# Kernel optimization log

Measured on AMD Instinct MI355X. Metric: run time of the kernel, lower is better.

Reference implementation:

```python
import jax
import jax.numpy as jnp
import numpy as np

B, L = 64, 128


def _lse(x, axis):
    # -inf-safe logsumexp; mirrors the torch code's NaN-masking autograd hooks
    m = jax.lax.stop_gradient(jnp.max(x, axis=axis, keepdims=True))
    m = jnp.where(jnp.isfinite(m), m, 0.0)
    s = jnp.sum(jnp.exp(x - m), axis=axis)
    out = jnp.log(jnp.where(s > 0, s, 1.0)) + jnp.squeeze(m, axis=axis)
    return jnp.where(s > 0, out, -jnp.inf)


def _inside(scores_p, lens):
    # scores_p: [L, L, B] == torch scores.permute(2, 1, 0); Eisner inside algorithm
    L_, _, Bn = scores_p.shape
    ar = jnp.arange(L_)
    ninf = jnp.array(-jnp.inf, scores_p.dtype)
    s_i = jnp.full((L_, L_, Bn), -jnp.inf, scores_p.dtype)  # incomplete spans
    s_c = jnp.full((L_, L_, Bn), -jnp.inf, scores_p.dtype)  # complete spans
    s_c = s_c.at[ar, ar].set(0.0)

    def step(carry, w):
        s_i, s_c = carry
        i = ar[:, None]                      # span start
        j = ar[None, :]                      # split offset
        valid = (j < w) & (i < L_ - w)       # [L, L] stripe mask for width w
        clip = lambda x: jnp.clip(x, 0, L_ - 1)
        vi = (ar < L_ - w)[:, None]          # valid span starts, [L, 1]
        lo, hi = clip(ar + w), ar            # diagonal coords (i+w, i)

        # incomplete: I(i<->i+w) = lse_r C(i, i+r) + C(i+w, i+r+1)  (stripe + stripe(w,1))
        ilr = s_c[clip(i), clip(i + j)] + s_c[clip(i + w), clip(i + j + 1)]
        il = _lse(jnp.where(valid[..., None], ilr, ninf), 1)       # [L, B]
        s_i = s_i.at[lo, hi].set(jnp.where(vi, il + scores_p[lo, hi], s_i[lo, hi]))
        s_i = s_i.at[hi, lo].set(jnp.where(vi, il + scores_p[hi, lo], s_i[hi, lo]))

        # complete left: C(i+w -> i) = lse_r C(i+r, i) + I(i+w, i+r)
        cl = s_c[clip(i + j), clip(i)] + s_i[clip(i + w), clip(i + j)]
        clv = _lse(jnp.where(valid[..., None], cl, ninf), 1)
        s_c = s_c.at[lo, hi].set(jnp.where(vi, clv, s_c[lo, hi]))

        # complete right: C(i -> i+w) = lse_r I(i, i+r+1) + C(i+r+1, i+w)
        cr = s_i[clip(i), clip(i + j + 1)] + s_c[clip(i + j + 1), clip(i + w)]
        crv = _lse(jnp.where(valid[..., None], cr, ninf), 1)
        # root span (0, w) is only valid for sentences of exactly length w
        crv = crv.at[0].set(jnp.where(lens == w, crv[0], ninf))
        s_c = s_c.at[hi, lo].set(jnp.where(vi, crv, s_c[hi, lo]))
        return (s_i, s_c), None

    (s_i, s_c), _ = jax.lax.scan(jax.checkpoint(step), (s_i, s_c), jnp.arange(1, L_))
    return s_i, s_c


def setup_inputs() -> dict:
    key = jax.random.key(0)
    k1, k2, k3 = jax.random.split(key, 3)
    scores = jax.random.normal(k1, (B, L, L), jnp.float32)
    lens = jax.random.randint(k2, (B,), L // 2, L)                 # sentence lengths
    pos = jnp.arange(L)
    mask = (pos[None, :] >= 1) & (pos[None, :] <= lens[:, None])   # prefix mask, mask.sum(1)==lens
    target = jax.random.randint(k3, (B, L), 0, L)
    target = jnp.minimum(target, lens[:, None])                    # gold heads inside sentence
    return {"scores": scores, "mask": mask, "target": target}


def reference(scores, mask, target):
    Bn, L_, _ = scores.shape
    lens = mask.sum(1)
    total = mask.sum().astype(scores.dtype)
    s_i, s_c = _inside(jnp.transpose(scores, (2, 1, 0)), lens)
    logZ = s_c[0, lens, jnp.arange(Bn)].sum()
    gold = jnp.take_along_axis(scores, target[..., None], axis=-1)[..., 0]
    loss = (logZ - jnp.where(mask, gold, jnp.zeros((), scores.dtype)).sum()) / total
    return loss
```

## Files before the change

kernel.cpp:

```cpp
#include <hip/hip_runtime.h>
#include <math.h>

#define LL 128
#define LP 129
#define TCR 132
#define TC_SZ (TCR * LP)
#define TI_SZ (LL * LP + 160)
#define NT 512
#define NW 8

#define LOG2E 1.4426950408889634f
#define LN2   0.6931471805599453f

template <int CTRL>
__device__ __forceinline__ float dppq(float v) {
  return __int_as_float(__builtin_amdgcn_update_dpp(
      0, __float_as_int(v), CTRL, 0xF, 0xF, true));
}
__device__ __forceinline__ float qmax(float v) {
  v = fmaxf(v, dppq<0xB1>(v));
  v = fmaxf(v, dppq<0x4E>(v));
  return v;
}
__device__ __forceinline__ float qsum(float v) {
  v += dppq<0xB1>(v);
  v += dppq<0x4E>(v);
  return v;
}

template <int K>
__device__ __forceinline__ void fusedPhase(
    float* __restrict__ tC, float* __restrict__ tI, const float* __restrict__ S,
    const int ii, const int w, const int jg, const bool writer,
    const bool rootBad, float (&paR)[32], float (&a1R)[32], float (&c1R)[32]) {
  const float sUp = S[ii * LL + ii + w];
  const float sLo = S[(ii + w) * LL + ii];
  const float* pb = tC + (ii + w) * LP + ii + 1 + jg;
  const float* a2 = tI + (ii + w) * LP + ii + jg;
  const float* c2 = tC + (ii + 1 + jg) * LP + ii + w;

  float vb[K], va[K], vc[K];
#pragma unroll
  for (int k = 0; k < K; ++k) vb[k] = pb[4 * k];
#pragma unroll
  for (int k = 0; k < K; ++k) va[k] = a2[4 * k];
#pragma unroll
  for (int k = 0; k < K; ++k) vc[k] = c2[4 * k * LP];

  float mA0 = -INFINITY, mA1 = -INFINITY;
#pragma unroll
  for (int k = 0; k < K; ++k) {
    float x = paR[k] + vb[k];
    if (k & 1) mA1 = fmaxf(mA1, x); else mA0 = fmaxf(mA0, x);
  }
  const float mA = qmax(fmaxf(mA0, mA1));
  const float msA = fmaxf(mA, -1e37f);
  const float nA = -msA * LOG2E;
  float sA0 = 0.f, sA1 = 0.f;
#pragma unroll
  for (int k = 0; k < K; ++k) {
    float e = __builtin_amdgcn_exp2f(
        __builtin_fmaf(paR[k] + vb[k], LOG2E, nA));
    if (k & 1) sA1 += e; else sA0 += e;
  }
  const float il = __builtin_amdgcn_logf(qsum(sA0 + sA1)) * LN2 + msA;

  float mL0 = -INFINITY, mL1 = -INFINITY;
#pragma unroll
  for (int k = 0; k < K; ++k) {
    float x = a1R[k] + va[k];
    if (k & 1) mL1 = fmaxf(mL1, x); else mL0 = fmaxf(mL0, x);
  }
  const float mL = qmax(fmaxf(mL0, mL1));
  const float msL = fmaxf(mL, -1e37f);
  const float nL = -msL * LOG2E;
  float sL0 = 0.f, sL1 = 0.f;
#pragma unroll
  for (int k = 0; k < K; ++k) {
    float e = __builtin_amdgcn_exp2f(
        __builtin_fmaf(a1R[k] + va[k], LOG2E, nL));
    if (k & 1) sL1 += e; else sL0 += e;
  }
  const float SL = qsum(sL0 + sL1);

  float mR0 = -INFINITY, mR1 = -INFINITY;
#pragma unroll
  for (int k = 0; k < K; ++k) {
    float x = c1R[k] + vc[k];
    if (k & 1) mR1 = fmaxf(mR1, x); else mR0 = fmaxf(mR0, x);
  }
  const float mR = qmax(fmaxf(mR0, mR1));
  const float msR = fmaxf(mR, -1e37f);
  const float nR = -msR * LOG2E;
  float sR0 = 0.f, sR1 = 0.f;
#pragma unroll
  for (int k = 0; k < K; ++k) {
    float e = __builtin_amdgcn_exp2f(
        __builtin_fmaf(c1R[k] + vc[k], LOG2E, nR));
    if (k & 1) sR1 += e; else sR0 += e;
  }
  const float SR = qsum(sR0 + sR1);

  const float t0 = il + sUp;
  const float tW = il + sLo;
  const float msfL = fmaxf(fmaxf(mL, t0), -1e37f);
  const float SLf = SL * __builtin_amdgcn_exp2f((msL - msfL) * LOG2E)
                  + __builtin_amdgcn_exp2f((t0 - msfL) * LOG2E);
  const float clv = __builtin_amdgcn_logf(SLf) * LN2 + msfL;
  const float msfR = fmaxf(fmaxf(mR, tW), -1e37f);
  const float SRf = SR * __builtin_amdgcn_exp2f((msR - msfR) * LOG2E)
                  + __builtin_amdgcn_exp2f((tW - msfR) * LOG2E);
  float crv = __builtin_amdgcn_logf(SRf) * LN2 + msfR;
  if (rootBad) crv = -INFINITY;

  if (writer) {
    tI[(ii + w) * LP + ii] = t0;
    tI[ii * LP + (ii + w)] = tW;
    tC[(ii + w) * LP + ii] = clv;
    tC[ii * LP + (ii + w)] = crv;
  }

  const int wm3 = w & 3;
  const bool lnw = (jg == wm3) && (wm3 != 0);
  paR[K - 1] = lnw ? crv : paR[K - 1];
  a1R[K - 1] = lnw ? clv : a1R[K - 1];
  if constexpr (K < 32) {
    const bool z = (jg == 0) && (wm3 == 0);
    paR[K] = z ? crv : paR[K];
    a1R[K] = z ? clv : a1R[K];
  }
  const bool ln1 = (jg == ((w - 1) & 3));
  c1R[K - 1] = ln1 ? tW : c1R[K - 1];
}

__global__ __launch_bounds__(NT, 2) void crf_inside(
    const float* __restrict__ scores, const int* __restrict__ mask,
    const int* __restrict__ target, float* __restrict__ acc) {
  extern __shared__ float lds[];
  float* tC = lds;
  float* tI = lds + TC_SZ;
  const int b = blockIdx.x;
  const int t = threadIdx.x;
  const int lane = t & 63;
  const int wv = t >> 6;
  const int r = lane >> 2;
  const int jg = lane & 3;
  const float* S = scores + (size_t)b * LL * LL;

  __shared__ float gred[NW];
  __shared__ int lred[NW];
  __shared__ float s_gold;
  __shared__ int s_len;

  int mv = 0; float gv = 0.f;
  if (t < LL) {
    mv = mask[b * LL + t] ? 1 : 0;
    if (mv) gv = S[t * LL + target[b * LL + t]];
  }
  int lm = mv; float lg = gv;
#pragma unroll
  for (int o = 32; o > 0; o >>= 1) {
    lm += __shfl_xor(lm, o, 64);
    lg += __shfl_xor(lg, o, 64);
  }
  if (lane == 0) { lred[wv] = lm; gred[wv] = lg; }

  for (int idx = t; idx < TC_SZ + TI_SZ; idx += NT) lds[idx] = -INFINITY;
  __syncthreads();
  if (t < LL) tC[t * LP + t] = 0.f;
  if (t == 0) {
    int l = 0; float g = 0.f;
    for (int k = 0; k < NW; ++k) { l += lred[k]; g += gred[k]; }
    s_len = l; s_gold = g;
  }
  __syncthreads();
  const int len = s_len;

  const int i = (wv << 4) + r;

  float paR[32], a1R[32], c1R[32];
#pragma unroll
  for (int k = 0; k < 32; ++k) { paR[k] = -INFINITY; a1R[k] = -INFINITY; c1R[k] = -INFINITY; }
  if (jg == 0) paR[0] = 0.f;

  for (int w = 1; w < LL; ++w) {
    const int ni = LL - w;
    const bool waveAct = (wv << 4) < ni;
    const int ii = min(i, ni - 1);
    const bool writer = (jg == 0) & (i < ni);
    const bool rootBad = (ii == 0) && (w != len);
    const int K = (w + 3) >> 2;
    if (waveAct) {
      switch (K) {
#define CASE_K(KK) case KK: fusedPhase<KK>(tC, tI, S, ii, w, jg, writer, rootBad, paR, a1R, c1R); break;
        CASE_K(1) CASE_K(2) CASE_K(3) CASE_K(4) CASE_K(5) CASE_K(6)
        CASE_K(7) CASE_K(8) CASE_K(9) CASE_K(10) CASE_K(11) CASE_K(12)
        CASE_K(13) CASE_K(14) CASE_K(15) CASE_K(16) CASE_K(17) CASE_K(18)
        CASE_K(19) CASE_K(20) CASE_K(21) CASE_K(22) CASE_K(23) CASE_K(24)
        CASE_K(25) CASE_K(26) CASE_K(27) CASE_K(28) CASE_K(29) CASE_K(30)
        CASE_K(31) CASE_K(32)
#undef CASE_K
      }
    }
    __syncthreads();
  }

  if (t == 0) {
    float logZ = tC[len];
    atomicAdd(&acc[0], logZ - s_gold);
    atomicAdd(&acc[1], (float)len);
  }
}

__global__ void zero_acc(float* acc) {
  acc[0] = 0.f;
  acc[1] = 0.f;
}

__global__ void finalize(const float* __restrict__ acc, float* __restrict__ out) {
  out[0] = acc[0] / acc[1];
}

extern "C" void kernel_launch(void* const* d_in, const int* in_sizes, int n_in,
                              void* d_out, int out_size, void* d_ws, size_t ws_size,
                              hipStream_t stream) {
  const float* scores = (const float*)d_in[0];
  const int* mask = (const int*)d_in[1];
  const int* target = (const int*)d_in[2];
  float* out = (float*)d_out;
  float* acc = (float*)d_ws;

  const int Bn = in_sizes[0] / (LL * LL);
  const size_t lds_bytes = (size_t)(TC_SZ + TI_SZ) * sizeof(float);

  (void)hipFuncSetAttribute((const void*)crf_inside,
                            hipFuncAttributeMaxDynamicSharedMemorySize,
                            (int)lds_bytes);

  zero_acc<<<1, 1, 0, stream>>>(acc);
  crf_inside<<<Bn, NT, lds_bytes, stream>>>(scores, mask, target, acc);
  finalize<<<1, 1, 0, stream>>>(acc, out);
}
```

Before: 255.6 us.

## Remap wide spans to larger thread groups and shrink register-cached stripes

For span widths above 64, the Eisner inside loop now assigns 8, 16, or 32 lanes per span instead of 4, reading all operands from LDS and reducing with ds_swizzle. Register caches of stripe values shrink from 32 to 17 entries per array, which lowers register pressure. The goal is to recover idle threads as the number of spans drops at large widths and to shorten the per-thread reduction length. The trade-off is more LDS reads and swizzle-based cross-lane reductions in the wide phase, plus a larger padded tC buffer.

Result: slower. 267.6 us (+4.7%).

```diff
diff --git a/kernel.cpp b/kernel.cpp
--- a/kernel.cpp
+++ b/kernel.cpp
@@ -3,7 +3,7 @@
 
 #define LL 128
 #define LP 129
-#define TCR 132
+#define TCR 144
 #define TC_SZ (TCR * LP)
 #define TI_SZ (LL * LP + 160)
 #define NT 512
@@ -27,12 +27,33 @@
   v += dppq<0x4E>(v);
   return v;
 }
+template <int MASK>
+__device__ __forceinline__ float swz(float v) {
+  return __int_as_float(__builtin_amdgcn_ds_swizzle(
+      __float_as_int(v), (MASK << 10) | 0x1F));
+}
+template <int G>
+__device__ __forceinline__ float gmaxr(float v) {
+  v = qmax(v);
+  if constexpr (G >= 8)  v = fmaxf(v, swz<4>(v));
+  if constexpr (G >= 16) v = fmaxf(v, swz<8>(v));
+  if constexpr (G >= 32) v = fmaxf(v, swz<16>(v));
+  return v;
+}
+template <int G>
+__device__ __forceinline__ float gsumr(float v) {
+  v = qsum(v);
+  if constexpr (G >= 8)  v += swz<4>(v);
+  if constexpr (G >= 16) v += swz<8>(v);
+  if constexpr (G >= 32) v += swz<16>(v);
+  return v;
+}
 
 template <int K>
 __device__ __forceinline__ void fusedPhase(
     float* __restrict__ tC, float* __restrict__ tI, const float* __restrict__ S,
     const int ii, const int w, const int jg, const bool writer,
-    const bool rootBad, float (&paR)[32], float (&a1R)[32], float (&c1R)[32]) {
+    const bool rootBad, float (&paR)[17], float (&a1R)[17], float (&c1R)[17]) {
   const float sUp = S[ii * LL + ii + w];
   const float sLo = S[(ii + w) * LL + ii];
   const float* pb = tC + (ii + w) * LP + ii + 1 + jg;
@@ -53,14 +74,12 @@
     float x = paR[k] + vb[k];
     if (k & 1) mA1 = fmaxf(mA1, x); else mA0 = fmaxf(mA0, x);
   }
-  const float mA = qmax(fmaxf(mA0, mA1));
-  const float msA = fmaxf(mA, -1e37f);
+  const float msA = fmaxf(qmax(fmaxf(mA0, mA1)), -1e37f);
   const float nA = -msA * LOG2E;
   float sA0 = 0.f, sA1 = 0.f;
 #pragma unroll
   for (int k = 0; k < K; ++k) {
-    float e = __builtin_amdgcn_exp2f(
-        __builtin_fmaf(paR[k] + vb[k], LOG2E, nA));
+    float e = __builtin_amdgcn_exp2f(__builtin_fmaf(paR[k] + vb[k], LOG2E, nA));
     if (k & 1) sA1 += e; else sA0 += e;
   }
   const float il = __builtin_amdgcn_logf(qsum(sA0 + sA1)) * LN2 + msA;
@@ -77,8 +96,7 @@
   float sL0 = 0.f, sL1 = 0.f;
 #pragma unroll
   for (int k = 0; k < K; ++k) {
-    float e = __builtin_amdgcn_exp2f(
-        __builtin_fmaf(a1R[k] + va[k], LOG2E, nL));
+    float e = __builtin_amdgcn_exp2f(__builtin_fmaf(a1R[k] + va[k], LOG2E, nL));
     if (k & 1) sL1 += e; else sL0 += e;
   }
   const float SL = qsum(sL0 + sL1);
@@ -95,8 +113,7 @@
   float sR0 = 0.f, sR1 = 0.f;
 #pragma unroll
   for (int k = 0; k < K; ++k) {
-    float e = __builtin_amdgcn_exp2f(
-        __builtin_fmaf(c1R[k] + vc[k], LOG2E, nR));
+    float e = __builtin_amdgcn_exp2f(__builtin_fmaf(c1R[k] + vc[k], LOG2E, nR));
     if (k & 1) sR1 += e; else sR0 += e;
   }
   const float SR = qsum(sR0 + sR1);
@@ -124,13 +141,111 @@
   const bool lnw = (jg == wm3) && (wm3 != 0);
   paR[K - 1] = lnw ? crv : paR[K - 1];
   a1R[K - 1] = lnw ? clv : a1R[K - 1];
-  if constexpr (K < 32) {
+  if constexpr (K < 16) {
     const bool z = (jg == 0) && (wm3 == 0);
     paR[K] = z ? crv : paR[K];
     a1R[K] = z ? clv : a1R[K];
+  } else {
+    const bool z = (jg == 0) && (wm3 == 0);
+    paR[16] = z ? crv : paR[16];
+    a1R[16] = z ? clv : a1R[16];
   }
   const bool ln1 = (jg == ((w - 1) & 3));
   c1R[K - 1] = ln1 ? tW : c1R[K - 1];
+}
+
+template <int G, int KG>
+__device__ __forceinline__ void widePhase(
+    float* __restrict__ tC, float* __restrict__ tI, const float* __restrict__ S,
+    const int ii, const int w, const int jgg, const bool writer,
+    const bool rootBad) {
+  const float sUp = S[ii * LL + ii + w];
+  const float sLo = S[(ii + w) * LL + ii];
+  const float* pa = tC + ii * LP + ii + jgg;
+  const float* pb = tC + (ii + w) * LP + ii + 1 + jgg;
+  const float* a1 = tC + (ii + jgg) * LP + ii;
+  const float* a2 = tI + (ii + w) * LP + ii + jgg;
+  const float* c1 = tI + ii * LP + ii + 1 + jgg;
+  const float* c2 = tC + (ii + 1 + jgg) * LP + ii + w;
+
+  float xa[KG], xl[KG], xr[KG];
+  const unsigned uw = (unsigned)w, uw1 = (unsigned)(w - 1);
+#pragma unroll
+  for (int k = 0; k < KG; ++k) {
+    float va_ = pa[G * k] + pb[G * k];
+    float vl_ = a1[G * k * LP] + a2[G * k];
+    float vr_ = c1[G * k] + c2[G * k * LP];
+    const unsigned j = (unsigned)(jgg + G * k);
+    xa[k] = (j < uw) ? va_ : -INFINITY;
+    xl[k] = (j - 1u < uw1) ? vl_ : -INFINITY;
+    xr[k] = (j < uw1) ? vr_ : -INFINITY;
+  }
+
+  float mA0 = -INFINITY, mA1 = -INFINITY;
+#pragma unroll
+  for (int k = 0; k < KG; ++k) {
+    if (k & 1) mA1 = fmaxf(mA1, xa[k]); else mA0 = fmaxf(mA0, xa[k]);
+  }
+  const float msA = fmaxf(gmaxr<G>(fmaxf(mA0, mA1)), -1e37f);
+  const float nA = -msA * LOG2E;
+  float sA0 = 0.f, sA1 = 0.f;
+#pragma unroll
+  for (int k = 0; k < KG; ++k) {
+    float e = __builtin_amdgcn_exp2f(__builtin_fmaf(xa[k], LOG2E, nA));
+    if (k & 1) sA1 += e; else sA0 += e;
+  }
+  const float il = __builtin_amdgcn_logf(gsumr<G>(sA0 + sA1)) * LN2 + msA;
+
+  float mL0 = -INFINITY, mL1 = -INFINITY;
+#pragma unroll
+  for (int k = 0; k < KG; ++k) {
+    if (k & 1) mL1 = fmaxf(mL1, xl[k]); else mL0 = fmaxf(mL0, xl[k]);
+  }
+  const float mL = gmaxr<G>(fmaxf(mL0, mL1));
+  const float msL = fmaxf(mL, -1e37f);
+  const float nL = -msL * LOG2E;
+  float sL0 = 0.f, sL1 = 0.f;
+#pragma unroll
+  for (int k = 0; k < KG; ++k) {
+    float e = __builtin_amdgcn_exp2f(__builtin_fmaf(xl[k], LOG2E, nL));
+    if (k & 1) sL1 += e; else sL0 += e;
+  }
+  const float SL = gsumr<G>(sL0 + sL1);
+
+  float mR0 = -INFINITY, mR1 = -INFINITY;
+#pragma unroll
+  for (int k = 0; k < KG; ++k) {
+    if (k & 1) mR1 = fmaxf(mR1, xr[k]); else mR0 = fmaxf(mR0, xr[k]);
+  }
+  const float mR = gmaxr<G>(fmaxf(mR0, mR1));
+  const float msR = fmaxf(mR, -1e37f);
+  const float nR = -msR * LOG2E;
+  float sR0 = 0.f, sR1 = 0.f;
+#pragma unroll
+  for (int k = 0; k < KG; ++k) {
+    float e = __builtin_amdgcn_exp2f(__builtin_fmaf(xr[k], LOG2E, nR));
+    if (k & 1) sR1 += e; else sR0 += e;
+  }
+  const float SR = gsumr<G>(sR0 + sR1);
+
+  const float t0 = il + sUp;
+  const float tW = il + sLo;
+  const float msfL = fmaxf(fmaxf(mL, t0), -1e37f);
+  const float SLf = SL * __builtin_amdgcn_exp2f((msL - msfL) * LOG2E)
+                  + __builtin_amdgcn_exp2f((t0 - msfL) * LOG2E);
+  const float clv = __builtin_amdgcn_logf(SLf) * LN2 + msfL;
+  const float msfR = fmaxf(fmaxf(mR, tW), -1e37f);
+  const float SRf = SR * __builtin_amdgcn_exp2f((msR - msfR) * LOG2E)
+                  + __builtin_amdgcn_exp2f((tW - msfR) * LOG2E);
+  float crv = __builtin_amdgcn_logf(SRf) * LN2 + msfR;
+  if (rootBad) crv = -INFINITY;
+
+  if (writer) {
+    tI[(ii + w) * LP + ii] = t0;
+    tI[ii * LP + (ii + w)] = tW;
+    tC[(ii + w) * LP + ii] = clv;
+    tC[ii * LP + (ii + w)] = crv;
+  }
 }
 
 __global__ __launch_bounds__(NT, 2) void crf_inside(
@@ -178,12 +293,12 @@
 
   const int i = (wv << 4) + r;
 
-  float paR[32], a1R[32], c1R[32];
-#pragma unroll
-  for (int k = 0; k < 32; ++k) { paR[k] = -INFINITY; a1R[k] = -INFINITY; c1R[k] = -INFINITY; }
+  float paR[17], a1R[17], c1R[17];
+#pragma unroll
+  for (int k = 0; k < 17; ++k) { paR[k] = -INFINITY; a1R[k] = -INFINITY; c1R[k] = -INFINITY; }
   if (jg == 0) paR[0] = 0.f;
 
-  for (int w = 1; w < LL; ++w) {
+  for (int w = 1; w <= 64; ++w) {
     const int ni = LL - w;
     const bool waveAct = (wv << 4) < ni;
     const int ii = min(i, ni - 1);
@@ -195,11 +310,43 @@
 #define CASE_K(KK) case KK: fusedPhase<KK>(tC, tI, S, ii, w, jg, writer, rootBad, paR, a1R, c1R); break;
         CASE_K(1) CASE_K(2) CASE_K(3) CASE_K(4) CASE_K(5) CASE_K(6)
         CASE_K(7) CASE_K(8) CASE_K(9) CASE_K(10) CASE_K(11) CASE_K(12)
-        CASE_K(13) CASE_K(14) CASE_K(15) CASE_K(16) CASE_K(17) CASE_K(18)
-        CASE_K(19) CASE_K(20) CASE_K(21) CASE_K(22) CASE_K(23) CASE_K(24)
-        CASE_K(25) CASE_K(26) CASE_K(27) CASE_K(28) CASE_K(29) CASE_K(30)
-        CASE_K(31) CASE_K(32)
+        CASE_K(13) CASE_K(14) CASE_K(15) CASE_K(16)
 #undef CASE_K
+      }
+    }
+    __syncthreads();
+  }
+
+  for (int w = 65; w < LL; ++w) {
+    const int ni = LL - w;
+    if (w <= 96) {
+      const int gi = t >> 3, jgg = t & 7;
+      if ((wv << 3) < ni) {
+        const int ii = min(gi, ni - 1);
+        const bool writer = (jgg == 0) & (gi < ni);
+        const bool rootBad = (ii == 0) && (w != len);
+        switch ((w + 7) >> 3) {
+          case 9:  widePhase<8, 9>(tC, tI, S, ii, w, jgg, writer, rootBad); break;
+          case 10: widePhase<8, 10>(tC, tI, S, ii, w, jgg, writer, rootBad); break;
+          case 11: widePhase<8, 11>(tC, tI, S, ii, w, jgg, writer, rootBad); break;
+          default: widePhase<8, 12>(tC, tI, S, ii, w, jgg, writer, rootBad); break;
+        }
+      }
+    } else if (w <= 112) {
+      const int gi = t >> 4, jgg = t & 15;
+      if ((wv << 2) < ni) {
+        const int ii = min(gi, ni - 1);
+        const bool writer = (jgg == 0) & (gi < ni);
+        const bool rootBad = (ii == 0) && (w != len);
+        widePhase<16, 7>(tC, tI, S, ii, w, jgg, writer, rootBad);
+      }
+    } else {
+      const int gi = t >> 5, jgg = t & 31;
+      if ((wv << 1) < ni) {
+        const int ii = min(gi, ni - 1);
+        const bool writer = (jgg == 0) & (gi < ni);
+        const bool rootBad = (ii == 0) && (w != len);
+        widePhase<32, 4>(tC, tI, S, ii, w, jgg, writer, rootBad);
       }
     }
     __syncthreads();
```

## Split each span reduction across 8 lanes with 1024-thread blocks

Applied to the files above, without the earlier changes.

Each span start now uses 8 lanes instead of 4 for its logsumexp reductions, and the block doubles to 1024 threads. The per-lane register arrays shrink from 32 to 16/17 entries, and the DPP reduction gains a third step (row shift) to combine 8 lanes. The load of the third operand is also moved later to lower register pressure. The goal is to halve the serial work per lane on each of the 127 dependent width steps, at the cost of an extra cross-lane step, more barrier participants and a larger LDS padding layout.

Measured after the change: 251.1 us. About the same (-1.8%).

```diff
diff --git a/kernel.cpp b/kernel.cpp
--- a/kernel.cpp
+++ b/kernel.cpp
@@ -3,11 +3,11 @@
 
 #define LL 128
 #define LP 129
-#define TCR 132
+#define TCR 136
 #define TC_SZ (TCR * LP)
-#define TI_SZ (LL * LP + 160)
-#define NT 512
-#define NW 8
+#define TI_SZ (LL * LP + 40)
+#define NT 1024
+#define NW 16
 
 #define LOG2E 1.4426950408889634f
 #define LN2   0.6931471805599453f
@@ -17,35 +17,35 @@
   return __int_as_float(__builtin_amdgcn_update_dpp(
       0, __float_as_int(v), CTRL, 0xF, 0xF, true));
 }
-__device__ __forceinline__ float qmax(float v) {
+__device__ __forceinline__ float g8max(float v) {
   v = fmaxf(v, dppq<0xB1>(v));
   v = fmaxf(v, dppq<0x4E>(v));
+  v = fmaxf(v, dppq<0x141>(v));
   return v;
 }
-__device__ __forceinline__ float qsum(float v) {
+__device__ __forceinline__ float g8sum(float v) {
   v += dppq<0xB1>(v);
   v += dppq<0x4E>(v);
+  v += dppq<0x141>(v);
   return v;
 }
 
 template <int K>
 __device__ __forceinline__ void fusedPhase(
     float* __restrict__ tC, float* __restrict__ tI, const float* __restrict__ S,
-    const int ii, const int w, const int jg, const bool writer,
-    const bool rootBad, float (&paR)[32], float (&a1R)[32], float (&c1R)[32]) {
+    const int ii, const int w, const int lg, const bool writer,
+    const bool rootBad, float (&paR)[17], float (&a1R)[17], float (&c1R)[16]) {
   const float sUp = S[ii * LL + ii + w];
   const float sLo = S[(ii + w) * LL + ii];
-  const float* pb = tC + (ii + w) * LP + ii + 1 + jg;
-  const float* a2 = tI + (ii + w) * LP + ii + jg;
-  const float* c2 = tC + (ii + 1 + jg) * LP + ii + w;
-
-  float vb[K], va[K], vc[K];
-#pragma unroll
-  for (int k = 0; k < K; ++k) vb[k] = pb[4 * k];
-#pragma unroll
-  for (int k = 0; k < K; ++k) va[k] = a2[4 * k];
-#pragma unroll
-  for (int k = 0; k < K; ++k) vc[k] = c2[4 * k * LP];
+  const float* pb = tC + (ii + w) * LP + ii + 1 + lg;
+  const float* a2 = tI + (ii + w) * LP + ii + lg;
+  const float* c2 = tC + (ii + 1 + lg) * LP + ii + w;
+
+  float vb[K], va[K];
+#pragma unroll
+  for (int k = 0; k < K; ++k) vb[k] = pb[8 * k];
+#pragma unroll
+  for (int k = 0; k < K; ++k) va[k] = a2[8 * k];
 
   float mA0 = -INFINITY, mA1 = -INFINITY;
 #pragma unroll
@@ -53,17 +53,15 @@
     float x = paR[k] + vb[k];
     if (k & 1) mA1 = fmaxf(mA1, x); else mA0 = fmaxf(mA0, x);
   }
-  const float mA = qmax(fmaxf(mA0, mA1));
-  const float msA = fmaxf(mA, -1e37f);
+  const float msA = fmaxf(g8max(fmaxf(mA0, mA1)), -1e37f);
   const float nA = -msA * LOG2E;
   float sA0 = 0.f, sA1 = 0.f;
 #pragma unroll
   for (int k = 0; k < K; ++k) {
-    float e = __builtin_amdgcn_exp2f(
-        __builtin_fmaf(paR[k] + vb[k], LOG2E, nA));
+    float e = __builtin_amdgcn_exp2f(__builtin_fmaf(paR[k] + vb[k], LOG2E, nA));
     if (k & 1) sA1 += e; else sA0 += e;
   }
-  const float il = __builtin_amdgcn_logf(qsum(sA0 + sA1)) * LN2 + msA;
+  const float il = __builtin_amdgcn_logf(g8sum(sA0 + sA1)) * LN2 + msA;
 
   float mL0 = -INFINITY, mL1 = -INFINITY;
 #pragma unroll
@@ -71,17 +69,20 @@
     float x = a1R[k] + va[k];
     if (k & 1) mL1 = fmaxf(mL1, x); else mL0 = fmaxf(mL0, x);
   }
-  const float mL = qmax(fmaxf(mL0, mL1));
+  const float mL = g8max(fmaxf(mL0, mL1));
   const float msL = fmaxf(mL, -1e37f);
   const float nL = -msL * LOG2E;
   float sL0 = 0.f, sL1 = 0.f;
 #pragma unroll
   for (int k = 0; k < K; ++k) {
-    float e = __builtin_amdgcn_exp2f(
-        __builtin_fmaf(a1R[k] + va[k], LOG2E, nL));
+    float e = __builtin_amdgcn_exp2f(__builtin_fmaf(a1R[k] + va[k], LOG2E, nL));
     if (k & 1) sL1 += e; else sL0 += e;
   }
-  const float SL = qsum(sL0 + sL1);
+  const float SL = g8sum(sL0 + sL1);
+
+  float vc[K];
+#pragma unroll
+  for (int k = 0; k < K; ++k) vc[k] = c2[8 * k * LP];
 
   float mR0 = -INFINITY, mR1 = -INFINITY;
 #pragma unroll
@@ -89,17 +90,16 @@
     float x = c1R[k] + vc[k];
     if (k & 1) mR1 = fmaxf(mR1, x); else mR0 = fmaxf(mR0, x);
   }
-  const float mR = qmax(fmaxf(mR0, mR1));
+  const float mR = g8max(fmaxf(mR0, mR1));
   const float msR = fmaxf(mR, -1e37f);
   const float nR = -msR * LOG2E;
   float sR0 = 0.f, sR1 = 0.f;
 #pragma unroll
   for (int k = 0; k < K; ++k) {
-    float e = __builtin_amdgcn_exp2f(
-        __builtin_fmaf(c1R[k] + vc[k], LOG2E, nR));
+    float e = __builtin_amdgcn_exp2f(__builtin_fmaf(c1R[k] + vc[k], LOG2E, nR));
     if (k & 1) sR1 += e; else sR0 += e;
   }
-  const float SR = qsum(sR0 + sR1);
+  const float SR = g8sum(sR0 + sR1);
 
   const float t0 = il + sUp;
   const float tW = il + sLo;
@@ -120,20 +120,20 @@
     tC[ii * LP + (ii + w)] = crv;
   }
 
-  const int wm3 = w & 3;
-  const bool lnw = (jg == wm3) && (wm3 != 0);
+  const int wm7 = w & 7;
+  const bool lnw = (lg == wm7) && (wm7 != 0);
   paR[K - 1] = lnw ? crv : paR[K - 1];
   a1R[K - 1] = lnw ? clv : a1R[K - 1];
-  if constexpr (K < 32) {
-    const bool z = (jg == 0) && (wm3 == 0);
+  if constexpr (K < 16) {
+    const bool z = (lg == 0) && (wm7 == 0);
     paR[K] = z ? crv : paR[K];
     a1R[K] = z ? clv : a1R[K];
   }
-  const bool ln1 = (jg == ((w - 1) & 3));
+  const bool ln1 = (lg == ((w - 1) & 7));
   c1R[K - 1] = ln1 ? tW : c1R[K - 1];
 }
 
-__global__ __launch_bounds__(NT, 2) void crf_inside(
+__global__ __launch_bounds__(NT, 4) void crf_inside(
     const float* __restrict__ scores, const int* __restrict__ mask,
     const int* __restrict__ target, float* __restrict__ acc) {
   extern __shared__ float lds[];
@@ -143,8 +143,8 @@
   const int t = threadIdx.x;
   const int lane = t & 63;
   const int wv = t >> 6;
-  const int r = lane >> 2;
-  const int jg = lane & 3;
+  const int g = t >> 3;
+  const int lg = t & 7;
   const float* S = scores + (size_t)b * LL * LL;
 
   __shared__ float gred[NW];
@@ -157,48 +157,45 @@
     mv = mask[b * LL + t] ? 1 : 0;
     if (mv) gv = S[t * LL + target[b * LL + t]];
   }
-  int lm = mv; float lg = gv;
+  int lm = mv; float lg_ = gv;
 #pragma unroll
   for (int o = 32; o > 0; o >>= 1) {
     lm += __shfl_xor(lm, o, 64);
-    lg += __shfl_xor(lg, o, 64);
-  }
-  if (lane == 0) { lred[wv] = lm; gred[wv] = lg; }
+    lg_ += __shfl_xor(lg_, o, 64);
+  }
+  if (lane == 0) { lred[wv] = lm; gred[wv] = lg_; }
 
   for (int idx = t; idx < TC_SZ + TI_SZ; idx += NT) lds[idx] = -INFINITY;
   __syncthreads();
   if (t < LL) tC[t * LP + t] = 0.f;
   if (t == 0) {
-    int l = 0; float g = 0.f;
-    for (int k = 0; k < NW; ++k) { l += lred[k]; g += gred[k]; }
-    s_len = l; s_gold = g;
+    int l = 0; float gg = 0.f;
+    for (int k = 0; k < NW; ++k) { l += lred[k]; gg += gred[k]; }
+    s_len = l; s_gold = gg;
   }
   __syncthreads();
   const int len = s_len;
 
-  const int i = (wv << 4) + r;
-
-  float paR[32], a1R[32], c1R[32];
-#pragma unroll
-  for (int k = 0; k < 32; ++k) { paR[k] = -INFINITY; a1R[k] = -INFINITY; c1R[k] = -INFINITY; }
-  if (jg == 0) paR[0] = 0.f;
+  float paR[17], a1R[17], c1R[16];
+#pragma unroll
+  for (int k = 0; k < 17; ++k) { paR[k] = -INFINITY; a1R[k] = -INFINITY; }
+#pragma unroll
+  for (int k = 0; k < 16; ++k) c1R[k] = -INFINITY;
+  if (lg == 0) paR[0] = 0.f;
 
   for (int w = 1; w < LL; ++w) {
     const int ni = LL - w;
-    const bool waveAct = (wv << 4) < ni;
-    const int ii = min(i, ni - 1);
-    const bool writer = (jg == 0) & (i < ni);
+    const bool waveAct = (wv << 3) < ni;
+    const int ii = min(g, ni - 1);
+    const bool writer = (lg == 0) & (g < ni);
     const bool rootBad = (ii == 0) && (w != len);
-    const int K = (w + 3) >> 2;
+    const int K = (w + 7) >> 3;
     if (waveAct) {
       switch (K) {
-#define CASE_K(KK) case KK: fusedPhase<KK>(tC, tI, S, ii, w, jg, writer, rootBad, paR, a1R, c1R); break;
+#define CASE_K(KK) case KK: fusedPhase<KK>(tC, tI, S, ii, w, lg, writer, rootBad, paR, a1R, c1R); break;
         CASE_K(1) CASE_K(2) CASE_K(3) CASE_K(4) CASE_K(5) CASE_K(6)
         CASE_K(7) CASE_K(8) CASE_K(9) CASE_K(10) CASE_K(11) CASE_K(12)
-        CASE_K(13) CASE_K(14) CASE_K(15) CASE_K(16) CASE_K(17) CASE_K(18)
-        CASE_K(19) CASE_K(20) CASE_K(21) CASE_K(22) CASE_K(23) CASE_K(24)
-        CASE_K(25) CASE_K(26) CASE_K(27) CASE_K(28) CASE_K(29) CASE_K(30)
-        CASE_K(31) CASE_K(32)
+        CASE_K(13) CASE_K(14) CASE_K(15) CASE_K(16)
 #undef CASE_K
       }
     }
```
